# Kernel tuning notes

Hardware: AMD Instinct MI355X
Metric: run time of the kernel (lower is better)

## Reference

```python
import jax, jax.numpy as jnp
import numpy as np

BS, SEQ, IN, H, L = 32, 512, 1024, 1024, 2
STDV = 1.0 / np.sqrt(H)


def setup_inputs() -> dict:
    key = jax.random.key(0)
    ks = jax.random.split(key, 5)
    # params are uniform(-stdv, stdv) per reset_parameters
    u = lambda k, shape: jax.random.uniform(k, shape, jnp.float32, -STDV, STDV)
    return {
        "x": jax.random.normal(ks[0], (BS, SEQ, IN), jnp.float32),
        "w_ih": u(ks[1], (L, H, IN)),   # layer 0: [H, IN]; layer >0 uses [H, H] (IN==H here)
        "w_hh": u(ks[2], (L, H, H)),
        "b_ih": u(ks[3], (L, H)),
        "b_hh": u(ks[4], (L, H)),
    }


def _run_layer(x_sbH, w_ih_l, w_hh_l, b_ih_l, b_hh_l):
    # x_sbH: [seq, bs, in]. Precompute input projection as one GEMM.
    xproj = jnp.einsum('sbi,hi->sbh', x_sbH, w_ih_l) + b_ih_l + b_hh_l  # [seq, bs, H]

    def step(h, xp_t):
        # h_t = tanh(W_ih x_t + b_ih + W_hh h_{t-1} + b_hh)
        h_new = jnp.tanh(xp_t + h @ w_hh_l.T)
        return h_new, h_new

    h0 = jnp.zeros((x_sbH.shape[1], w_hh_l.shape[0]), x_sbH.dtype)
    h_last, hs = jax.lax.scan(step, h0, xproj)
    return hs, h_last  # hs: [seq, bs, H]


def reference(x, w_ih, w_hh, b_ih, b_hh):
    # batch_first: transpose to [seq, bs, in]
    h = jnp.transpose(x, (1, 0, 2))
    finals = []
    num_layers = w_ih.shape[0]
    for l in range(num_layers):
        h, h_last = _run_layer(h, w_ih[l], w_hh[l], b_ih[l], b_hh[l])
        finals.append(h_last)
    output = jnp.transpose(h, (1, 0, 2))           # [bs, seq, H]
    h_n = jnp.stack(finals, axis=0)                # [num_layers, bs, H]
    return output, h_n
```

## Files before the change

kernel.cpp:

```cpp
#include <hip/hip_runtime.h>

#define SEQL 512
#define BSZ  32
#define HID  1024
#define NWG  48
#define HN_OFF 16777216

#define XPS_OFF 0u
#define H0B_OFF 67108864u
#define FLG_OFF 100663296u

using f32x4  = __attribute__((ext_vector_type(4))) float;
using u16x8  = __attribute__((ext_vector_type(8))) unsigned short;
using bf16x8 = __attribute__((ext_vector_type(8))) __bf16;
using u64x2  = __attribute__((ext_vector_type(2))) unsigned long long;

__device__ __forceinline__ f32x4 mfma16(u16x8 a, u16x8 b, f32x4 c) {
  return __builtin_amdgcn_mfma_f32_16x16x32_bf16(
      __builtin_bit_cast(bf16x8, a), __builtin_bit_cast(bf16x8, b), c, 0, 0, 0);
}

__device__ __forceinline__ unsigned short f2bf(float f) {
  unsigned u = __builtin_bit_cast(unsigned, f);
  u += 0x7fffu + ((u >> 16) & 1u);
  return (unsigned short)(u >> 16);
}

__device__ __forceinline__ float tanh_fast(float x) {
  float cx = fminf(fmaxf(x, -15.f), 15.f);
  float e = __expf(2.f * cx);
  return __fdividef(e - 1.f, e + 1.f);
}

__device__ __forceinline__ void stwt(unsigned long long* p, unsigned long long v) {
  __hip_atomic_store(p, v, __ATOMIC_RELAXED, __HIP_MEMORY_SCOPE_AGENT);
}
__device__ __forceinline__ unsigned long long ldat(const unsigned long long* p) {
  return __hip_atomic_load(p, __ATOMIC_RELAXED, __HIP_MEMORY_SCOPE_AGENT);
}
__device__ __forceinline__ unsigned ldat32(const unsigned* p) {
  return __hip_atomic_load(p, __ATOMIC_RELAXED, __HIP_MEMORY_SCOPE_AGENT);
}
__device__ __forceinline__ void stflag(unsigned* p) {
  __hip_atomic_store(p, 1u, __ATOMIC_RELAXED, __HIP_MEMORY_SCOPE_AGENT);
}

__device__ __forceinline__ void wave_wait4(const unsigned* flt, int w, int lane) {
  const unsigned long long* q = (const unsigned long long*)flt + 2 * w + (lane & 1);
  unsigned long long v;
  do {
    v = ldat(q);
  } while (!__all(((unsigned)v != 0u) & ((unsigned)(v >> 32) != 0u)));
}
__device__ __forceinline__ void wave_wait1(const unsigned* p) {
  while (!__all(ldat32(p) != 0u)) {}
}

__global__ void init_kernel(unsigned int* flg) {
  int i = blockIdx.x * 256 + threadIdx.x;
  flg[i] = 0u;
}

__global__ __launch_bounds__(256, 2)
void xproj_gemm(const float* __restrict__ X,
                const float* __restrict__ W,
                const float* __restrict__ bih,
                const float* __restrict__ bhh,
                float* __restrict__ out)
{
  __shared__ unsigned short sA[128 * 32];
  __shared__ unsigned short sB[128 * 32];
  const int tid  = threadIdx.x;
  const int lane = tid & 63;
  const int wave = tid >> 6;
  const int wm = wave >> 1, wn = wave & 1;
  const int bm = blockIdx.x >> 3;
  const int bn = blockIdx.x & 7;
  const int l15 = lane & 15;
  const int koff = (lane >> 4) * 8;
  const int srow = tid >> 2;
  const int skc  = (tid & 3) * 8;

  f32x4 acc[4][4];
#pragma unroll
  for (int i = 0; i < 4; ++i)
#pragma unroll
    for (int j = 0; j < 4; ++j) acc[i][j] = (f32x4)0.f;

  for (int k0 = 0; k0 < HID; k0 += 32) {
#pragma unroll
    for (int r = 0; r < 2; ++r) {
      int row = r * 64 + srow;
      int Mrow = bm * 128 + row;
      const float* src = X + ((size_t)(Mrow & 31) * SEQL + (Mrow >> 5)) * HID + k0 + skc;
      float4 a = ((const float4*)src)[0];
      float4 b = ((const float4*)src)[1];
      u16x8 av;
      av[0]=f2bf(a.x); av[1]=f2bf(a.y); av[2]=f2bf(a.z); av[3]=f2bf(a.w);
      av[4]=f2bf(b.x); av[5]=f2bf(b.y); av[6]=f2bf(b.z); av[7]=f2bf(b.w);
      *(u16x8*)&sA[row * 32 + skc] = av;

      const float* wsrc = W + (size_t)(bn * 128 + row) * HID + k0 + skc;
      float4 wa = ((const float4*)wsrc)[0];
      float4 wb = ((const float4*)wsrc)[1];
      u16x8 wv;
      wv[0]=f2bf(wa.x); wv[1]=f2bf(wa.y); wv[2]=f2bf(wa.z); wv[3]=f2bf(wa.w);
      wv[4]=f2bf(wb.x); wv[5]=f2bf(wb.y); wv[6]=f2bf(wb.z); wv[7]=f2bf(wb.w);
      *(u16x8*)&sB[row * 32 + skc] = wv;
    }
    __syncthreads();

    u16x8 af[4], bfr[4];
#pragma unroll
    for (int mt = 0; mt < 4; ++mt)
      af[mt] = *(const u16x8*)&sA[(wm * 64 + mt * 16 + l15) * 32 + koff];
#pragma unroll
    for (int nt = 0; nt < 4; ++nt)
      bfr[nt] = *(const u16x8*)&sB[(wn * 64 + nt * 16 + l15) * 32 + koff];
#pragma unroll
    for (int mt = 0; mt < 4; ++mt)
#pragma unroll
      for (int nt = 0; nt < 4; ++nt)
        acc[mt][nt] = mfma16(af[mt], bfr[nt], acc[mt][nt]);
    __syncthreads();
  }

#pragma unroll
  for (int nt = 0; nt < 4; ++nt) {
    int colg = bn * 128 + wn * 64 + nt * 16 + l15;
    float bias = bih[colg] + bhh[colg];
#pragma unroll
    for (int mt = 0; mt < 4; ++mt) {
#pragma unroll
      for (int i = 0; i < 4; ++i) {
        int rowg = bm * 128 + wm * 64 + mt * 16 + (lane >> 4) * 4 + i;
        out[(size_t)rowg * HID + colg] = acc[mt][nt][i] + bias;
      }
    }
  }
}

__global__ __launch_bounds__(256, 1)
void fused_scan(float* __restrict__ xps,
                const float* __restrict__ whh0,
                const float* __restrict__ wih1,
                const float* __restrict__ whh1,
                const float* __restrict__ bih1,
                const float* __restrict__ bhh1,
                unsigned short* __restrict__ h0b,
                float* __restrict__ out,
                unsigned int* __restrict__ flg)
{
  const int tid  = threadIdx.x;
  const int lane = tid & 63;
  const int wave = tid >> 6;
  const int l15  = lane & 15;
  const int l4   = lane >> 4;
  const int stage = blockIdx.x >> 4;
  const int wg    = blockIdx.x & 15;
  const int col0  = wg * 64;
  const int kbase = wave * 256;
  const int frow  = tid >> 3;
  const int fcb   = (tid & 7) * 8;

  unsigned* fl0 = flg;
  unsigned* fl1 = flg + SEQL * 16;
  unsigned* fl2 = flg + 2 * SEQL * 16;

  __shared__ float red[4][32][68];

  const float* Wsl = (stage == 0) ? whh0 : (stage == 1) ? wih1 : whh1;
  u16x8 Bf[4][8];
#pragma unroll
  for (int nt = 0; nt < 4; ++nt) {
#pragma unroll
    for (int ks = 0; ks < 8; ++ks) {
      const float* src = Wsl + (size_t)(col0 + nt * 16 + l15) * HID + kbase + ks * 32 + l4 * 8;
      float4 a = ((const float4*)src)[0];
      float4 b = ((const float4*)src)[1];
      u16x8 v;
      v[0]=f2bf(a.x); v[1]=f2bf(a.y); v[2]=f2bf(a.z); v[3]=f2bf(a.w);
      v[4]=f2bf(b.x); v[5]=f2bf(b.y); v[6]=f2bf(b.z); v[7]=f2bf(b.w);
      Bf[nt][ks] = v;
    }
  }

  if (stage == 0) {
    unsigned long long xpv[4];
    {
      const float* np = xps + (size_t)frow * HID + col0 + fcb;
#pragma unroll
      for (int p = 0; p < 4; ++p) xpv[p] = ldat((const unsigned long long*)np + p);
    }
    for (int t = 0; t < SEQL; ++t) {
      f32x4 acc[2][4];
#pragma unroll
      for (int m = 0; m < 2; ++m)
#pragma unroll
        for (int n = 0; n < 4; ++n) acc[m][n] = (f32x4)0.f;
      if (t > 0) {
        wave_wait4(fl0 + (t - 1) * 16, wave, lane);
        const unsigned short* hp = h0b + (size_t)(t - 1) * (BSZ * HID);
        u16x8 Af[2][8];
#pragma unroll
        for (int m = 0; m < 2; ++m)
#pragma unroll
          for (int ks = 0; ks < 8; ++ks)
            Af[m][ks] = *(const u16x8*)(hp + (size_t)(m * 16 + l15) * HID + kbase + ks * 32 + l4 * 8);
#pragma unroll
        for (int ks = 0; ks < 8; ++ks)
#pragma unroll
          for (int m = 0; m < 2; ++m)
#pragma unroll
            for (int n = 0; n < 4; ++n)
              acc[m][n] = mfma16(Af[m][ks], Bf[n][ks], acc[m][n]);
      }
#pragma unroll
      for (int m = 0; m < 2; ++m)
#pragma unroll
        for (int n = 0; n < 4; ++n)
#pragma unroll
          for (int q = 0; q < 4; ++q)
            red[wave][m * 16 + l4 * 4 + q][n * 16 + l15] = acc[m][n][q];
      __syncthreads();
      float sv[8];
#pragma unroll
      for (int jj = 0; jj < 2; ++jj) {
        float4 r0 = *(const float4*)&red[0][frow][fcb + jj * 4];
        float4 r1 = *(const float4*)&red[1][frow][fcb + jj * 4];
        float4 r2 = *(const float4*)&red[2][frow][fcb + jj * 4];
        float4 r3 = *(const float4*)&red[3][frow][fcb + jj * 4];
        sv[jj*4+0] = r0.x + r1.x + r2.x + r3.x;
        sv[jj*4+1] = r0.y + r1.y + r2.y + r3.y;
        sv[jj*4+2] = r0.z + r1.z + r2.z + r3.z;
        sv[jj*4+3] = r0.w + r1.w + r2.w + r3.w;
      }
      float hv[8];
#pragma unroll
      for (int p = 0; p < 4; ++p) {
        float2 f = __builtin_bit_cast(float2, xpv[p]);
        hv[2*p]   = tanh_fast(sv[2*p]   + f.x);
        hv[2*p+1] = tanh_fast(sv[2*p+1] + f.y);
      }
      u16x8 hb;
#pragma unroll
      for (int j = 0; j < 8; ++j) hb[j] = f2bf(hv[j]);
      u64x2 hq = __builtin_bit_cast(u64x2, hb);
      unsigned long long* hdst =
          (unsigned long long*)(h0b + (size_t)t * (BSZ * HID) + (size_t)frow * HID + col0 + fcb);
      stwt(hdst, hq[0]); stwt(hdst + 1, hq[1]);
      if (t == SEQL - 1) {
        float* o = out + HN_OFF + (size_t)frow * HID + col0 + fcb;
        ((float4*)o)[0] = make_float4(hv[0], hv[1], hv[2], hv[3]);
        ((float4*)o)[1] = make_float4(hv[4], hv[5], hv[6], hv[7]);
      } else {
        const float* np = xps + ((size_t)(t + 1) * BSZ + frow) * HID + col0 + fcb;
#pragma unroll
        for (int p = 0; p < 4; ++p) xpv[p] = ldat((const unsigned long long*)np + p);
      }
      asm volatile("s_waitcnt vmcnt(0)" ::: "memory");
      __syncthreads();
      if (tid == 0) stflag(&fl0[t * 16 + wg]);
    }
  } else if (stage == 1) {
    for (int t = 0; t < SEQL; ++t) {
      wave_wait4(fl0 + t * 16, wave, lane);
      const unsigned short* hp = h0b + (size_t)t * (BSZ * HID);
      u16x8 Af[2][8];
#pragma unroll
      for (int m = 0; m < 2; ++m)
#pragma unroll
        for (int ks = 0; ks < 8; ++ks)
          Af[m][ks] = *(const u16x8*)(hp + (size_t)(m * 16 + l15) * HID + kbase + ks * 32 + l4 * 8);
      f32x4 acc[2][4];
#pragma unroll
      for (int m = 0; m < 2; ++m)
#pragma unroll
        for (int n = 0; n < 4; ++n) acc[m][n] = (f32x4)0.f;
#pragma unroll
      for (int ks = 0; ks < 8; ++ks)
#pragma unroll
        for (int m = 0; m < 2; ++m)
#pragma unroll
          for (int n = 0; n < 4; ++n)
            acc[m][n] = mfma16(Af[m][ks], Bf[n][ks], acc[m][n]);
#pragma unroll
      for (int m = 0; m < 2; ++m)
#pragma unroll
        for (int n = 0; n < 4; ++n)
#pragma unroll
          for (int q = 0; q < 4; ++q)
            red[wave][m * 16 + l4 * 4 + q][n * 16 + l15] = acc[m][n][q];
      __syncthreads();
      float sv[8];
#pragma unroll
      for (int jj = 0; jj < 2; ++jj) {
        float4 r0 = *(const float4*)&red[0][frow][fcb + jj * 4];
        float4 r1 = *(const float4*)&red[1][frow][fcb + jj * 4];
        float4 r2 = *(const float4*)&red[2][frow][fcb + jj * 4];
        float4 r3 = *(const float4*)&red[3][frow][fcb + jj * 4];
        sv[jj*4+0] = r0.x + r1.x + r2.x + r3.x;
        sv[jj*4+1] = r0.y + r1.y + r2.y + r3.y;
        sv[jj*4+2] = r0.z + r1.z + r2.z + r3.z;
        sv[jj*4+3] = r0.w + r1.w + r2.w + r3.w;
      }
      float bia[8];
#pragma unroll
      for (int j = 0; j < 8; ++j)
        bia[j] = bih1[col0 + fcb + j] + bhh1[col0 + fcb + j];
      float* dst = xps + ((size_t)t * BSZ + frow) * HID + col0 + fcb;
#pragma unroll
      for (int p = 0; p < 4; ++p) {
        float2 f = make_float2(sv[2*p] + bia[2*p], sv[2*p+1] + bia[2*p+1]);
        stwt((unsigned long long*)dst + p, __builtin_bit_cast(unsigned long long, f));
      }
      asm volatile("s_waitcnt vmcnt(0)" ::: "memory");
      __syncthreads();
      if (tid == 0) stflag(&fl1[t * 16 + wg]);
    }
  } else {
    for (int t = 0; t < SEQL; ++t) {
      f32x4 acc[2][4];
#pragma unroll
      for (int m = 0; m < 2; ++m)
#pragma unroll
        for (int n = 0; n < 4; ++n) acc[m][n] = (f32x4)0.f;
      if (t > 0) {
        wave_wait4(fl2 + (t - 1) * 16, wave, lane);
        u16x8 Af[2][8];
#pragma unroll
        for (int m = 0; m < 2; ++m)
#pragma unroll
          for (int ks = 0; ks < 8; ++ks) {
            const float* src = out + ((size_t)(m * 16 + l15) * SEQL + (t - 1)) * HID + kbase + ks * 32 + l4 * 8;
            float4 a = ((const float4*)src)[0];
            float4 b = ((const float4*)src)[1];
            bf16x8 bv;
            bv[0]=(__bf16)a.x; bv[1]=(__bf16)a.y; bv[2]=(__bf16)a.z; bv[3]=(__bf16)a.w;
            bv[4]=(__bf16)b.x; bv[5]=(__bf16)b.y; bv[6]=(__bf16)b.z; bv[7]=(__bf16)b.w;
            Af[m][ks] = __builtin_bit_cast(u16x8, bv);
          }
#pragma unroll
        for (int ks = 0; ks < 8; ++ks)
#pragma unroll
          for (int m = 0; m < 2; ++m)
#pragma unroll
            for (int n = 0; n < 4; ++n)
              acc[m][n] = mfma16(Af[m][ks], Bf[n][ks], acc[m][n]);
      }
#pragma unroll
      for (int m = 0; m < 2; ++m)
#pragma unroll
        for (int n = 0; n < 4; ++n)
#pragma unroll
          for (int q = 0; q < 4; ++q)
            red[wave][m * 16 + l4 * 4 + q][n * 16 + l15] = acc[m][n][q];
      __syncthreads();
      wave_wait1(&fl1[t * 16 + wg]);
      const float* qp = xps + ((size_t)t * BSZ + frow) * HID + col0 + fcb;
      float4 q0 = ((const float4*)qp)[0];
      float4 q1 = ((const float4*)qp)[1];
      float sv[8];
#pragma unroll
      for (int jj = 0; jj < 2; ++jj) {
        float4 r0 = *(const float4*)&red[0][frow][fcb + jj * 4];
        float4 r1 = *(const float4*)&red[1][frow][fcb + jj * 4];
        float4 r2 = *(const float4*)&red[2][frow][fcb + jj * 4];
        float4 r3 = *(const float4*)&red[3][frow][fcb + jj * 4];
        sv[jj*4+0] = r0.x + r1.x + r2.x + r3.x;
        sv[jj*4+1] = r0.y + r1.y + r2.y + r3.y;
        sv[jj*4+2] = r0.z + r1.z + r2.z + r3.z;
        sv[jj*4+3] = r0.w + r1.w + r2.w + r3.w;
      }
      float xv[8] = {q0.x, q0.y, q0.z, q0.w, q1.x, q1.y, q1.z, q1.w};
      float hv[8];
#pragma unroll
      for (int j = 0; j < 8; ++j) hv[j] = tanh_fast(sv[j] + xv[j]);
      float* op = out + ((size_t)frow * SEQL + t) * HID + col0 + fcb;
#pragma unroll
      for (int p = 0; p < 4; ++p) {
        float2 f = make_float2(hv[2*p], hv[2*p+1]);
        stwt((unsigned long long*)op + p, __builtin_bit_cast(unsigned long long, f));
      }
      if (t == SEQL - 1) {
        float* o = out + HN_OFF + BSZ * HID + (size_t)frow * HID + col0 + fcb;
        ((float4*)o)[0] = make_float4(hv[0], hv[1], hv[2], hv[3]);
        ((float4*)o)[1] = make_float4(hv[4], hv[5], hv[6], hv[7]);
      }
      asm volatile("s_waitcnt vmcnt(0)" ::: "memory");
      __syncthreads();
      if (tid == 0) stflag(&fl2[t * 16 + wg]);
    }
  }
}

extern "C" void kernel_launch(void* const* d_in, const int* in_sizes, int n_in,
                              void* d_out, int out_size, void* d_ws, size_t ws_size,
                              hipStream_t stream) {
  const float* x    = (const float*)d_in[0];
  const float* w_ih = (const float*)d_in[1];
  const float* w_hh = (const float*)d_in[2];
  const float* b_ih = (const float*)d_in[3];
  const float* b_hh = (const float*)d_in[4];
  float* out = (float*)d_out;
  char* ws = (char*)d_ws;

  float* xps          = (float*)(ws + XPS_OFF);
  unsigned short* h0b = (unsigned short*)(ws + H0B_OFF);
  unsigned int* flg   = (unsigned int*)(ws + FLG_OFF);

  init_kernel<<<96, 256, 0, stream>>>(flg);
  xproj_gemm<<<1024, 256, 0, stream>>>(x, w_ih, b_ih, b_hh, xps);
  fused_scan<<<NWG, 256, 0, stream>>>(xps, w_hh,
      w_ih + (size_t)HID * HID, w_hh + (size_t)HID * HID,
      b_ih + HID, b_hh + HID, h0b, out, flg);
}
```

Baseline: 4.145 ms.

## Pin scan workgroups to one XCC and cut inter-stage traffic to half precision

The persistent scan kernel now launches 384 workgroups. Each one registers its XCC id through an atomic boot counter, and only the first XCC to collect 48 workgroups keeps them, so all producer/consumer flag and hidden-state exchange stays inside one XCC's L2. The input projection buffer becomes fp16, and layer-1 hidden state is also written as a bf16 side buffer, so the recurrent A-tile loads read half the bytes and skip fp32-to-bf16 conversion. Loads use inline sc0 asm instead of atomic loads. The changes add fp16 rounding of the pre-activations, rely on hardware XCC-id registers and co-residency assumptions, and add launch overhead for the idle workgroups.

```diff
diff --git a/kernel.cpp b/kernel.cpp
--- a/kernel.cpp
+++ b/kernel.cpp
@@ -3,17 +3,20 @@
 #define SEQL 512
 #define BSZ  32
 #define HID  1024
-#define NWG  48
+#define NWORK 48
+#define NLAUNCH 384
 #define HN_OFF 16777216
 
 #define XPS_OFF 0u
-#define H0B_OFF 67108864u
+#define H0B_OFF 33554432u
+#define H1B_OFF 67108864u
 #define FLG_OFF 100663296u
+#define BOOT_OFF 100794368u
 
 using f32x4  = __attribute__((ext_vector_type(4))) float;
 using u16x8  = __attribute__((ext_vector_type(8))) unsigned short;
+using u32x4  = __attribute__((ext_vector_type(4))) unsigned int;
 using bf16x8 = __attribute__((ext_vector_type(8))) __bf16;
-using u64x2  = __attribute__((ext_vector_type(2))) unsigned long long;
 
 __device__ __forceinline__ f32x4 mfma16(u16x8 a, u16x8 b, f32x4 c) {
   return __builtin_amdgcn_mfma_f32_16x16x32_bf16(
@@ -25,6 +28,13 @@
   u += 0x7fffu + ((u >> 16) & 1u);
   return (unsigned short)(u >> 16);
 }
+__device__ __forceinline__ unsigned short f2h(float f) {
+  _Float16 h = (_Float16)f;
+  return __builtin_bit_cast(unsigned short, h);
+}
+__device__ __forceinline__ float h2f(unsigned short u) {
+  return (float)__builtin_bit_cast(_Float16, u);
+}
 
 __device__ __forceinline__ float tanh_fast(float x) {
   float cx = fminf(fmaxf(x, -15.f), 15.f);
@@ -32,33 +42,63 @@
   return __fdividef(e - 1.f, e + 1.f);
 }
 
-__device__ __forceinline__ void stwt(unsigned long long* p, unsigned long long v) {
-  __hip_atomic_store(p, v, __ATOMIC_RELAXED, __HIP_MEMORY_SCOPE_AGENT);
-}
-__device__ __forceinline__ unsigned long long ldat(const unsigned long long* p) {
+__device__ __forceinline__ void ld_tile_sc0(const unsigned short* base, u32x4 (&r)[16]) {
+  const char* b0 = (const char*)base;
+  const char* b1 = b0 + 16 * HID * 2;
+  asm volatile(
+    "global_load_dwordx4 %0, %16, off sc0\n\t"
+    "global_load_dwordx4 %1, %16, off offset:64 sc0\n\t"
+    "global_load_dwordx4 %2, %16, off offset:128 sc0\n\t"
+    "global_load_dwordx4 %3, %16, off offset:192 sc0\n\t"
+    "global_load_dwordx4 %4, %16, off offset:256 sc0\n\t"
+    "global_load_dwordx4 %5, %16, off offset:320 sc0\n\t"
+    "global_load_dwordx4 %6, %16, off offset:384 sc0\n\t"
+    "global_load_dwordx4 %7, %16, off offset:448 sc0\n\t"
+    "global_load_dwordx4 %8, %17, off sc0\n\t"
+    "global_load_dwordx4 %9, %17, off offset:64 sc0\n\t"
+    "global_load_dwordx4 %10, %17, off offset:128 sc0\n\t"
+    "global_load_dwordx4 %11, %17, off offset:192 sc0\n\t"
+    "global_load_dwordx4 %12, %17, off offset:256 sc0\n\t"
+    "global_load_dwordx4 %13, %17, off offset:320 sc0\n\t"
+    "global_load_dwordx4 %14, %17, off offset:384 sc0\n\t"
+    "global_load_dwordx4 %15, %17, off offset:448 sc0\n\t"
+    "s_waitcnt vmcnt(0)"
+    : "=&v"(r[0]), "=&v"(r[1]), "=&v"(r[2]), "=&v"(r[3]),
+      "=&v"(r[4]), "=&v"(r[5]), "=&v"(r[6]), "=&v"(r[7]),
+      "=&v"(r[8]), "=&v"(r[9]), "=&v"(r[10]), "=&v"(r[11]),
+      "=&v"(r[12]), "=&v"(r[13]), "=&v"(r[14]), "=&v"(r[15])
+    : "v"(b0), "v"(b1)
+    : "memory");
+}
+
+__device__ __forceinline__ u16x8 ld8h_sc0(const void* p) {
+  u32x4 r;
+  asm volatile("global_load_dwordx4 %0, %1, off sc0\n\ts_waitcnt vmcnt(0)"
+               : "=&v"(r) : "v"(p) : "memory");
+  return __builtin_bit_cast(u16x8, r);
+}
+
+__device__ __forceinline__ void flag_set(unsigned* p) {
+  __hip_atomic_store(p, 1u, __ATOMIC_RELAXED, __HIP_MEMORY_SCOPE_AGENT);
+}
+__device__ __forceinline__ unsigned flag_get(const unsigned* p) {
   return __hip_atomic_load(p, __ATOMIC_RELAXED, __HIP_MEMORY_SCOPE_AGENT);
 }
-__device__ __forceinline__ unsigned ldat32(const unsigned* p) {
-  return __hip_atomic_load(p, __ATOMIC_RELAXED, __HIP_MEMORY_SCOPE_AGENT);
-}
-__device__ __forceinline__ void stflag(unsigned* p) {
-  __hip_atomic_store(p, 1u, __ATOMIC_RELAXED, __HIP_MEMORY_SCOPE_AGENT);
-}
-
-__device__ __forceinline__ void wave_wait4(const unsigned* flt, int w, int lane) {
-  const unsigned long long* q = (const unsigned long long*)flt + 2 * w + (lane & 1);
-  unsigned long long v;
-  do {
-    v = ldat(q);
-  } while (!__all(((unsigned)v != 0u) & ((unsigned)(v >> 32) != 0u)));
+__device__ __forceinline__ void wave_wait4(const unsigned* flt, int wave, int lane) {
+  const unsigned* p = flt + wave * 4 + (lane & 3);
+  while (!__all(flag_get(p) != 0u)) {}
 }
 __device__ __forceinline__ void wave_wait1(const unsigned* p) {
-  while (!__all(ldat32(p) != 0u)) {}
-}
-
-__global__ void init_kernel(unsigned int* flg) {
+  while (!__all(flag_get(p) != 0u)) {}
+}
+
+__global__ void init_kernel(unsigned* flg, int* boot) {
   int i = blockIdx.x * 256 + threadIdx.x;
   flg[i] = 0u;
+  if (blockIdx.x == 0) {
+    if (threadIdx.x < 16) boot[threadIdx.x] = 0;
+    if (threadIdx.x == 16) boot[16] = -1;
+  }
 }
 
 __global__ __launch_bounds__(256, 2)
@@ -66,7 +106,7 @@
                 const float* __restrict__ W,
                 const float* __restrict__ bih,
                 const float* __restrict__ bhh,
-                float* __restrict__ out)
+                unsigned short* __restrict__ out)
 {
   __shared__ unsigned short sA[128 * 32];
   __shared__ unsigned short sB[128 * 32];
@@ -134,45 +174,71 @@
 #pragma unroll
       for (int i = 0; i < 4; ++i) {
         int rowg = bm * 128 + wm * 64 + mt * 16 + (lane >> 4) * 4 + i;
-        out[(size_t)rowg * HID + colg] = acc[mt][nt][i] + bias;
+        out[(size_t)rowg * HID + colg] = f2h(acc[mt][nt][i] + bias);
       }
     }
   }
 }
 
-__global__ __launch_bounds__(256, 1)
-void fused_scan(float* __restrict__ xps,
+__global__ __launch_bounds__(256, 2)
+void fused_scan(unsigned short* __restrict__ xps,
                 const float* __restrict__ whh0,
                 const float* __restrict__ wih1,
                 const float* __restrict__ whh1,
                 const float* __restrict__ bih1,
                 const float* __restrict__ bhh1,
                 unsigned short* __restrict__ h0b,
+                unsigned short* __restrict__ h1b,
                 float* __restrict__ out,
-                unsigned int* __restrict__ flg)
+                unsigned* __restrict__ flg,
+                int* __restrict__ boot)
 {
   const int tid  = threadIdx.x;
+
+  __shared__ int s_role;
+  if (tid == 0) {
+    unsigned xcc;
+    asm volatile("s_getreg_b32 %0, hwreg(HW_REG_XCC_ID)" : "=s"(xcc));
+    xcc &= 15u;
+    int slot = __hip_atomic_fetch_add(&boot[(int)xcc], 1, __ATOMIC_RELAXED,
+                                      __HIP_MEMORY_SCOPE_AGENT);
+    if (slot == NWORK - 1) {
+      int exp = -1;
+      __hip_atomic_compare_exchange_strong(&boot[16], &exp, (int)xcc,
+          __ATOMIC_RELAXED, __ATOMIC_RELAXED, __HIP_MEMORY_SCOPE_AGENT);
+    }
+    int ch;
+    while ((ch = __hip_atomic_load(&boot[16], __ATOMIC_RELAXED,
+                                   __HIP_MEMORY_SCOPE_AGENT)) < 0)
+      __builtin_amdgcn_s_sleep(8);
+    s_role = ((int)xcc == ch && slot < NWORK) ? slot : -1;
+  }
+  __syncthreads();
+  const int role = s_role;
+  if (role < 0) return;
+
   const int lane = tid & 63;
   const int wave = tid >> 6;
   const int l15  = lane & 15;
   const int l4   = lane >> 4;
-  const int stage = blockIdx.x >> 4;
-  const int wg    = blockIdx.x & 15;
+  const int stage = role >> 4;
+  const int wg    = role & 15;
   const int col0  = wg * 64;
   const int kbase = wave * 256;
   const int frow  = tid >> 3;
   const int fcb   = (tid & 7) * 8;
-
-  unsigned* fl0 = flg;
-  unsigned* fl1 = flg + SEQL * 16;
-  unsigned* fl2 = flg + 2 * SEQL * 16;
+  const int laneoff = l15 * HID + kbase + l4 * 8;
+
+  unsigned* flA = flg;
+  unsigned* flB = flg + SEQL * 16;
+  unsigned* flC = flg + 2 * SEQL * 16;
 
   __shared__ float red[4][32][68];
 
   const float* Wsl = (stage == 0) ? whh0 : (stage == 1) ? wih1 : whh1;
   u16x8 Bf[4][8];
 #pragma unroll
-  for (int nt = 0; nt < 4; ++nt) {
+  for (int nt = 0; nt < 4; ++nt)
 #pragma unroll
     for (int ks = 0; ks < 8; ++ks) {
       const float* src = Wsl + (size_t)(col0 + nt * 16 + l15) * HID + kbase + ks * 32 + l4 * 8;
@@ -183,15 +249,9 @@
       v[4]=f2bf(b.x); v[5]=f2bf(b.y); v[6]=f2bf(b.z); v[7]=f2bf(b.w);
       Bf[nt][ks] = v;
     }
-  }
 
   if (stage == 0) {
-    unsigned long long xpv[4];
-    {
-      const float* np = xps + (size_t)frow * HID + col0 + fcb;
-#pragma unroll
-      for (int p = 0; p < 4; ++p) xpv[p] = ldat((const unsigned long long*)np + p);
-    }
+    u16x8 xh = *(const u16x8*)(xps + (size_t)frow * HID + col0 + fcb);
     for (int t = 0; t < SEQL; ++t) {
       f32x4 acc[2][4];
 #pragma unroll
@@ -199,22 +259,75 @@
 #pragma unroll
         for (int n = 0; n < 4; ++n) acc[m][n] = (f32x4)0.f;
       if (t > 0) {
-        wave_wait4(fl0 + (t - 1) * 16, wave, lane);
-        const unsigned short* hp = h0b + (size_t)(t - 1) * (BSZ * HID);
-        u16x8 Af[2][8];
+        wave_wait4(flA + (t - 1) * 16, wave, lane);
+        u32x4 r[16];
+        ld_tile_sc0(h0b + (size_t)(t - 1) * (BSZ * HID) + laneoff, r);
+#pragma unroll
+        for (int ks = 0; ks < 8; ++ks)
+#pragma unroll
+          for (int m = 0; m < 2; ++m)
+#pragma unroll
+            for (int n = 0; n < 4; ++n)
+              acc[m][n] = mfma16(__builtin_bit_cast(u16x8, r[m * 8 + ks]), Bf[n][ks], acc[m][n]);
+      }
+#pragma unroll
+      for (int m = 0; m < 2; ++m)
+#pragma unroll
+        for (int n = 0; n < 4; ++n)
+#pragma unroll
+          for (int q = 0; q < 4; ++q)
+            red[wave][m * 16 + l4 * 4 + q][n * 16 + l15] = acc[m][n][q];
+      __syncthreads();
+      float hv[8];
+#pragma unroll
+      for (int jj = 0; jj < 2; ++jj) {
+        float4 r0 = *(const float4*)&red[0][frow][fcb + jj * 4];
+        float4 r1 = *(const float4*)&red[1][frow][fcb + jj * 4];
+        float4 r2 = *(const float4*)&red[2][frow][fcb + jj * 4];
+        float4 r3 = *(const float4*)&red[3][frow][fcb + jj * 4];
+        hv[jj*4+0] = r0.x + r1.x + r2.x + r3.x;
+        hv[jj*4+1] = r0.y + r1.y + r2.y + r3.y;
+        hv[jj*4+2] = r0.z + r1.z + r2.z + r3.z;
+        hv[jj*4+3] = r0.w + r1.w + r2.w + r3.w;
+      }
+#pragma unroll
+      for (int j = 0; j < 8; ++j) hv[j] = tanh_fast(hv[j] + h2f((unsigned short)xh[j]));
+      u16x8 hb;
+#pragma unroll
+      for (int j = 0; j < 8; ++j) hb[j] = f2bf(hv[j]);
+      *(u16x8*)(h0b + (size_t)t * (BSZ * HID) + (size_t)frow * HID + col0 + fcb) = hb;
+      if (t == SEQL - 1) {
+        float* o = out + HN_OFF + (size_t)frow * HID + col0 + fcb;
+        ((float4*)o)[0] = make_float4(hv[0], hv[1], hv[2], hv[3]);
+        ((float4*)o)[1] = make_float4(hv[4], hv[5], hv[6], hv[7]);
+      } else {
+        xh = *(const u16x8*)(xps + ((size_t)(t + 1) * BSZ + frow) * HID + col0 + fcb);
+      }
+      asm volatile("s_waitcnt vmcnt(0)" ::: "memory");
+      __syncthreads();
+      if (tid == 0) flag_set(&flA[t * 16 + wg]);
+    }
+  } else if (stage == 1) {
+    float bia[8];
+#pragma unroll
+    for (int j = 0; j < 8; ++j)
+      bia[j] = bih1[col0 + fcb + j] + bhh1[col0 + fcb + j];
+    for (int t = 0; t < SEQL; ++t) {
+      wave_wait4(flA + t * 16, wave, lane);
+      u32x4 r[16];
+      ld_tile_sc0(h0b + (size_t)t * (BSZ * HID) + laneoff, r);
+      f32x4 acc[2][4];
+#pragma unroll
+      for (int m = 0; m < 2; ++m)
+#pragma unroll
+        for (int n = 0; n < 4; ++n) acc[m][n] = (f32x4)0.f;
+#pragma unroll
+      for (int ks = 0; ks < 8; ++ks)
 #pragma unroll
         for (int m = 0; m < 2; ++m)
 #pragma unroll
-          for (int ks = 0; ks < 8; ++ks)
-            Af[m][ks] = *(const u16x8*)(hp + (size_t)(m * 16 + l15) * HID + kbase + ks * 32 + l4 * 8);
-#pragma unroll
-        for (int ks = 0; ks < 8; ++ks)
-#pragma unroll
-          for (int m = 0; m < 2; ++m)
-#pragma unroll
-            for (int n = 0; n < 4; ++n)
-              acc[m][n] = mfma16(Af[m][ks], Bf[n][ks], acc[m][n]);
-      }
+          for (int n = 0; n < 4; ++n)
+            acc[m][n] = mfma16(__builtin_bit_cast(u16x8, r[m * 8 + ks]), Bf[n][ks], acc[m][n]);
 #pragma unroll
       for (int m = 0; m < 2; ++m)
 #pragma unroll
@@ -235,55 +348,33 @@
         sv[jj*4+2] = r0.z + r1.z + r2.z + r3.z;
         sv[jj*4+3] = r0.w + r1.w + r2.w + r3.w;
       }
-      float hv[8];
-#pragma unroll
-      for (int p = 0; p < 4; ++p) {
-        float2 f = __builtin_bit_cast(float2, xpv[p]);
-        hv[2*p]   = tanh_fast(sv[2*p]   + f.x);
-        hv[2*p+1] = tanh_fast(sv[2*p+1] + f.y);
-      }
-      u16x8 hb;
-#pragma unroll
-      for (int j = 0; j < 8; ++j) hb[j] = f2bf(hv[j]);
-      u64x2 hq = __builtin_bit_cast(u64x2, hb);
-      unsigned long long* hdst =
-          (unsigned long long*)(h0b + (size_t)t * (BSZ * HID) + (size_t)frow * HID + col0 + fcb);
-      stwt(hdst, hq[0]); stwt(hdst + 1, hq[1]);
-      if (t == SEQL - 1) {
-        float* o = out + HN_OFF + (size_t)frow * HID + col0 + fcb;
-        ((float4*)o)[0] = make_float4(hv[0], hv[1], hv[2], hv[3]);
-        ((float4*)o)[1] = make_float4(hv[4], hv[5], hv[6], hv[7]);
-      } else {
-        const float* np = xps + ((size_t)(t + 1) * BSZ + frow) * HID + col0 + fcb;
-#pragma unroll
-        for (int p = 0; p < 4; ++p) xpv[p] = ldat((const unsigned long long*)np + p);
-      }
+      u16x8 xo;
+#pragma unroll
+      for (int j = 0; j < 8; ++j) xo[j] = f2h(sv[j] + bia[j]);
+      *(u16x8*)(xps + ((size_t)t * BSZ + frow) * HID + col0 + fcb) = xo;
       asm volatile("s_waitcnt vmcnt(0)" ::: "memory");
       __syncthreads();
-      if (tid == 0) stflag(&fl0[t * 16 + wg]);
-    }
-  } else if (stage == 1) {
+      if (tid == 0) flag_set(&flB[t * 16 + wg]);
+    }
+  } else {
     for (int t = 0; t < SEQL; ++t) {
-      wave_wait4(fl0 + t * 16, wave, lane);
-      const unsigned short* hp = h0b + (size_t)t * (BSZ * HID);
-      u16x8 Af[2][8];
-#pragma unroll
-      for (int m = 0; m < 2; ++m)
+      f32x4 acc[2][4];
+#pragma unroll
+      for (int m = 0; m < 2; ++m)
+#pragma unroll
+        for (int n = 0; n < 4; ++n) acc[m][n] = (f32x4)0.f;
+      if (t > 0) {
+        wave_wait4(flC + (t - 1) * 16, wave, lane);
+        u32x4 r[16];
+        ld_tile_sc0(h1b + (size_t)(t - 1) * (BSZ * HID) + laneoff, r);
 #pragma unroll
         for (int ks = 0; ks < 8; ++ks)
-          Af[m][ks] = *(const u16x8*)(hp + (size_t)(m * 16 + l15) * HID + kbase + ks * 32 + l4 * 8);
-      f32x4 acc[2][4];
-#pragma unroll
-      for (int m = 0; m < 2; ++m)
-#pragma unroll
-        for (int n = 0; n < 4; ++n) acc[m][n] = (f32x4)0.f;
-#pragma unroll
-      for (int ks = 0; ks < 8; ++ks)
-#pragma unroll
-        for (int m = 0; m < 2; ++m)
-#pragma unroll
-          for (int n = 0; n < 4; ++n)
-            acc[m][n] = mfma16(Af[m][ks], Bf[n][ks], acc[m][n]);
+#pragma unroll
+          for (int m = 0; m < 2; ++m)
+#pragma unroll
+            for (int n = 0; n < 4; ++n)
+              acc[m][n] = mfma16(__builtin_bit_cast(u16x8, r[m * 8 + ks]), Bf[n][ks], acc[m][n]);
+      }
 #pragma unroll
       for (int m = 0; m < 2; ++m)
 #pragma unroll
@@ -292,96 +383,29 @@
           for (int q = 0; q < 4; ++q)
             red[wave][m * 16 + l4 * 4 + q][n * 16 + l15] = acc[m][n][q];
       __syncthreads();
-      float sv[8];
+      wave_wait1(&flB[t * 16 + wg]);
+      u16x8 xq = ld8h_sc0(xps + ((size_t)t * BSZ + frow) * HID + col0 + fcb);
+      float hv[8];
 #pragma unroll
       for (int jj = 0; jj < 2; ++jj) {
         float4 r0 = *(const float4*)&red[0][frow][fcb + jj * 4];
         float4 r1 = *(const float4*)&red[1][frow][fcb + jj * 4];
         float4 r2 = *(const float4*)&red[2][frow][fcb + jj * 4];
         float4 r3 = *(const float4*)&red[3][frow][fcb + jj * 4];
-        sv[jj*4+0] = r0.x + r1.x + r2.x + r3.x;
-        sv[jj*4+1] = r0.y + r1.y + r2.y + r3.y;
-        sv[jj*4+2] = r0.z + r1.z + r2.z + r3.z;
-        sv[jj*4+3] = r0.w + r1.w + r2.w + r3.w;
-      }
-      float bia[8];
-#pragma unroll
-      for (int j = 0; j < 8; ++j)
-        bia[j] = bih1[col0 + fcb + j] + bhh1[col0 + fcb + j];
-      float* dst = xps + ((size_t)t * BSZ + frow) * HID + col0 + fcb;
-#pragma unroll
-      for (int p = 0; p < 4; ++p) {
-        float2 f = make_float2(sv[2*p] + bia[2*p], sv[2*p+1] + bia[2*p+1]);
-        stwt((unsigned long long*)dst + p, __builtin_bit_cast(unsigned long long, f));
-      }
-      asm volatile("s_waitcnt vmcnt(0)" ::: "memory");
-      __syncthreads();
-      if (tid == 0) stflag(&fl1[t * 16 + wg]);
-    }
-  } else {
-    for (int t = 0; t < SEQL; ++t) {
-      f32x4 acc[2][4];
-#pragma unroll
-      for (int m = 0; m < 2; ++m)
-#pragma unroll
-        for (int n = 0; n < 4; ++n) acc[m][n] = (f32x4)0.f;
-      if (t > 0) {
-        wave_wait4(fl2 + (t - 1) * 16, wave, lane);
-        u16x8 Af[2][8];
-#pragma unroll
-        for (int m = 0; m < 2; ++m)
-#pragma unroll
-          for (int ks = 0; ks < 8; ++ks) {
-            const float* src = out + ((size_t)(m * 16 + l15) * SEQL + (t - 1)) * HID + kbase + ks * 32 + l4 * 8;
-            float4 a = ((const float4*)src)[0];
-            float4 b = ((const float4*)src)[1];
-            bf16x8 bv;
-            bv[0]=(__bf16)a.x; bv[1]=(__bf16)a.y; bv[2]=(__bf16)a.z; bv[3]=(__bf16)a.w;
-            bv[4]=(__bf16)b.x; bv[5]=(__bf16)b.y; bv[6]=(__bf16)b.z; bv[7]=(__bf16)b.w;
-            Af[m][ks] = __builtin_bit_cast(u16x8, bv);
-          }
-#pragma unroll
-        for (int ks = 0; ks < 8; ++ks)
-#pragma unroll
-          for (int m = 0; m < 2; ++m)
-#pragma unroll
-            for (int n = 0; n < 4; ++n)
-              acc[m][n] = mfma16(Af[m][ks], Bf[n][ks], acc[m][n]);
-      }
-#pragma unroll
-      for (int m = 0; m < 2; ++m)
-#pragma unroll
-        for (int n = 0; n < 4; ++n)
-#pragma unroll
-          for (int q = 0; q < 4; ++q)
-            red[wave][m * 16 + l4 * 4 + q][n * 16 + l15] = acc[m][n][q];
-      __syncthreads();
-      wave_wait1(&fl1[t * 16 + wg]);
-      const float* qp = xps + ((size_t)t * BSZ + frow) * HID + col0 + fcb;
-      float4 q0 = ((const float4*)qp)[0];
-      float4 q1 = ((const float4*)qp)[1];
-      float sv[8];
-#pragma unroll
-      for (int jj = 0; jj < 2; ++jj) {
-        float4 r0 = *(const float4*)&red[0][frow][fcb + jj * 4];
-        float4 r1 = *(const float4*)&red[1][frow][fcb + jj * 4];
-        float4 r2 = *(const float4*)&red[2][frow][fcb + jj * 4];
-        float4 r3 = *(const float4*)&red[3][frow][fcb + jj * 4];
-        sv[jj*4+0] = r0.x + r1.x + r2.x + r3.x;
-        sv[jj*4+1] = r0.y + r1.y + r2.y + r3.y;
-        sv[jj*4+2] = r0.z + r1.z + r2.z + r3.z;
-        sv[jj*4+3] = r0.w + r1.w + r2.w + r3.w;
-      }
-      float xv[8] = {q0.x, q0.y, q0.z, q0.w, q1.x, q1.y, q1.z, q1.w};
-      float hv[8];
-#pragma unroll
-      for (int j = 0; j < 8; ++j) hv[j] = tanh_fast(sv[j] + xv[j]);
+        hv[jj*4+0] = r0.x + r1.x + r2.x + r3.x;
+        hv[jj*4+1] = r0.y + r1.y + r2.y + r3.y;
+        hv[jj*4+2] = r0.z + r1.z + r2.z + r3.z;
+        hv[jj*4+3] = r0.w + r1.w + r2.w + r3.w;
+      }
+#pragma unroll
+      for (int j = 0; j < 8; ++j) hv[j] = tanh_fast(hv[j] + h2f((unsigned short)xq[j]));
+      u16x8 hb;
+#pragma unroll
+      for (int j = 0; j < 8; ++j) hb[j] = f2bf(hv[j]);
+      *(u16x8*)(h1b + (size_t)t * (BSZ * HID) + (size_t)frow * HID + col0 + fcb) = hb;
       float* op = out + ((size_t)frow * SEQL + t) * HID + col0 + fcb;
-#pragma unroll
-      for (int p = 0; p < 4; ++p) {
-        float2 f = make_float2(hv[2*p], hv[2*p+1]);
-        stwt((unsigned long long*)op + p, __builtin_bit_cast(unsigned long long, f));
-      }
+      ((float4*)op)[0] = make_float4(hv[0], hv[1], hv[2], hv[3]);
+      ((float4*)op)[1] = make_float4(hv[4], hv[5], hv[6], hv[7]);
       if (t == SEQL - 1) {
         float* o = out + HN_OFF + BSZ * HID + (size_t)frow * HID + col0 + fcb;
         ((float4*)o)[0] = make_float4(hv[0], hv[1], hv[2], hv[3]);
@@ -389,7 +413,7 @@
       }
       asm volatile("s_waitcnt vmcnt(0)" ::: "memory");
       __syncthreads();
-      if (tid == 0) stflag(&fl2[t * 16 + wg]);
+      if (tid == 0) flag_set(&flC[t * 16 + wg]);
     }
   }
 }
@@ -405,13 +429,15 @@
   float* out = (float*)d_out;
   char* ws = (char*)d_ws;
 
-  float* xps          = (float*)(ws + XPS_OFF);
+  unsigned short* xps = (unsigned short*)(ws + XPS_OFF);
   unsigned short* h0b = (unsigned short*)(ws + H0B_OFF);
-  unsigned int* flg   = (unsigned int*)(ws + FLG_OFF);
-
-  init_kernel<<<96, 256, 0, stream>>>(flg);
+  unsigned short* h1b = (unsigned short*)(ws + H1B_OFF);
+  unsigned* flg       = (unsigned*)(ws + FLG_OFF);
+  int* boot           = (int*)(ws + BOOT_OFF);
+
+  init_kernel<<<96, 256, 0, stream>>>(flg, boot);
   xproj_gemm<<<1024, 256, 0, stream>>>(x, w_ih, b_ih, b_hh, xps);
-  fused_scan<<<NWG, 256, 0, stream>>>(xps, w_hh,
+  fused_scan<<<NLAUNCH, 256, 0, stream>>>(xps, w_hh,
       w_ih + (size_t)HID * HID, w_hh + (size_t)HID * HID,
-      b_ih + HID, b_hh + HID, h0b, out, flg);
-}
+      b_ih + HID, b_hh + HID, h0b, h1b, out, flg, boot);
+}
```

Measured after the change: 3.788 ms. -8.6%, faster.
